# Performance work log

Hardware: AMD Instinct MI355X
Metric: run time of the kernel (lower is better)

## Reference

```python
import jax, jax.numpy as jnp
import numpy as np


def setup_inputs() -> dict:
    key = jax.random.key(0)
    k1, k2 = jax.random.split(key)
    B, L1, L2, D = 8, 2048, 2048, 1024
    features_1 = jax.random.normal(k1, (B, L1, D), dtype=jnp.float32)
    features_2 = jax.random.normal(k2, (B, L2, D), dtype=jnp.float32)
    return {"features_1": features_1, "features_2": features_2}


def reference(features_1, features_2):
    # similarity: [B, L1, L2], no scaling (matches original)
    sim = jnp.einsum("bmd,bnd->bmn", features_1, features_2)
    # both softmaxes in the original are dim=-1 (row softmax over L2)
    attn = jax.nn.softmax(sim, axis=-1)  # [B, L1, L2]
    attended_1 = jnp.einsum("bmn,bnd->bmd", attn, features_2)   # [B, L1, D]
    attended_2 = jnp.einsum("bmn,bmd->bnd", attn, features_1)   # attn^T @ f1 -> [B, L2, D]
    return (attended_1, attended_2)
```

## Files before the change

### kernel.cpp

```cpp
#include <hip/hip_runtime.h>
#include <hip/hip_fp16.h>

#define LDIM 2048
#define DDIM 1024
#define NB 8

typedef __attribute__((ext_vector_type(8))) _Float16 f16x8;
typedef __attribute__((ext_vector_type(4))) float f32x4;
typedef unsigned int u32;

#define MFMA16(a, b, c) __builtin_amdgcn_mfma_f32_16x16x32_f16(a, b, c, 0, 0, 0)

typedef const __attribute__((address_space(1))) u32* gas_t;
typedef __attribute__((address_space(3))) u32* las_t;

__device__ __forceinline__ void gl16(const _Float16* g, _Float16* l) {
  __builtin_amdgcn_global_load_lds((gas_t)g, (las_t)l, 16, 0, 0);
}

#define SBAR() __builtin_amdgcn_s_barrier()
#define VMCNT(n) asm volatile("s_waitcnt vmcnt(" #n ")" ::: "memory")
#define LGKM0 asm volatile("s_waitcnt lgkmcnt(0)" ::: "memory")
#define SCHED0 __builtin_amdgcn_sched_barrier(0)

template <int MH, int KS, int BB, class FS, class FW>
__device__ __forceinline__ void phase(const _Float16* sh, int base_a, int base_b,
                                      f32x4 (&acc)[2][4][4], FS stg, FW wt) {
  f16x8 af[4], bf[4];
#pragma unroll
  for (int mr = 0; mr < 4; ++mr)
    af[mr] = *(const f16x8*)&sh[BB * 32768 + KS * 8192 + MH * 2048 + base_a + mr * 512];
#pragma unroll
  for (int nr = 0; nr < 4; ++nr)
    bf[nr] = *(const f16x8*)&sh[BB * 32768 + 16384 + KS * 8192 + base_b + nr * 512];
  stg();
  wt();
  __builtin_amdgcn_s_barrier();
  LGKM0;
  SCHED0;
  __builtin_amdgcn_s_setprio(1);
#pragma unroll
  for (int mr = 0; mr < 4; ++mr)
#pragma unroll
    for (int nr = 0; nr < 4; ++nr)
      acc[MH][mr][nr] = MFMA16(af[mr], bf[nr], acc[MH][mr][nr]);
  __builtin_amdgcn_s_setprio(0);
  SCHED0;
  __builtin_amdgcn_s_barrier();
}

template <int LDA, int NT>
__device__ __forceinline__ void gemm8(const _Float16* __restrict__ Ab,
                                      const _Float16* __restrict__ Bb,
                                      _Float16* sh, f32x4 (&acc)[2][4][4]) {
  const int tid = threadIdx.x;
  const int lane = tid & 63, w = tid >> 6;
  const int wm = w >> 2, wn = w & 3;
  const int l15 = lane & 15, g4 = lane >> 4;

  const int sw = (l15 >> 1) & 3;
  const int chk = (g4 ^ sw) << 3;
  const int base_a = (wm * 128 + l15) * 32 + chk;
  const int base_b = (wn * 64 + l15) * 32 + chk;

  const int srow = tid >> 2;
  const int scg = (tid & 3) ^ ((srow >> 1) & 3);
  const _Float16* gA = Ab + (size_t)srow * LDA + scg * 8;
  const _Float16* gB = Bb + (size_t)srow * LDA + scg * 8;
  _Float16* lw = sh + w * 512;

  auto stgA = [&](int kt, int kh, int tb) {
    const _Float16* g = gA + (size_t)kt * 64 + kh * 32;
    _Float16* l = lw + tb * 32768 + kh * 8192;
    gl16(g, l);
    gl16(g + (size_t)128 * LDA, l + 4096);
  };
  auto stgB = [&](int kt, int kh, int tb) {
    const _Float16* g = gB + (size_t)kt * 64 + kh * 32;
    _Float16* l = lw + tb * 32768 + 16384 + kh * 8192;
    gl16(g, l);
    gl16(g + (size_t)128 * LDA, l + 4096);
  };

  stgA(0, 0, 0); stgB(0, 0, 0);
  stgA(0, 1, 0); stgB(0, 1, 0);
  stgA(1, 0, 1); stgB(1, 0, 1);
  VMCNT(8);
  SBAR();

  for (int t = 0; t + 3 < NT; t += 2) {
    phase<0, 0, 0>(sh, base_a, base_b, acc, [&] { stgA(t + 1, 1, 1); }, [] {});
    phase<1, 0, 0>(sh, base_a, base_b, acc, [&] { stgB(t + 1, 1, 1); }, [] { VMCNT(8); });
    phase<0, 1, 0>(sh, base_a, base_b, acc, [&] { stgA(t + 2, 0, 0); }, [] {});
    phase<1, 1, 0>(sh, base_a, base_b, acc, [&] { stgB(t + 2, 0, 0); }, [] { VMCNT(8); });
    phase<0, 0, 1>(sh, base_a, base_b, acc, [&] { stgA(t + 2, 1, 0); }, [] {});
    phase<1, 0, 1>(sh, base_a, base_b, acc, [&] { stgB(t + 2, 1, 0); }, [] { VMCNT(8); });
    phase<0, 1, 1>(sh, base_a, base_b, acc, [&] { stgA(t + 3, 0, 1); }, [] {});
    phase<1, 1, 1>(sh, base_a, base_b, acc, [&] { stgB(t + 3, 0, 1); }, [] { VMCNT(8); });
  }
  constexpr int T = NT - 2;
  phase<0, 0, 0>(sh, base_a, base_b, acc, [&] { stgA(T + 1, 1, 1); }, [] {});
  phase<1, 0, 0>(sh, base_a, base_b, acc, [&] { stgB(T + 1, 1, 1); }, [] { VMCNT(8); });
  phase<0, 1, 0>(sh, base_a, base_b, acc, [] {}, [] {});
  phase<1, 1, 0>(sh, base_a, base_b, acc, [] {}, [] { VMCNT(4); });
  phase<0, 0, 1>(sh, base_a, base_b, acc, [] {}, [] {});
  phase<1, 0, 1>(sh, base_a, base_b, acc, [] {}, [] { VMCNT(0); });
  phase<0, 1, 1>(sh, base_a, base_b, acc, [] {}, [] {});
  phase<1, 1, 1>(sh, base_a, base_b, acc, [] {}, [] {});
}

__global__ __launch_bounds__(256)
void k_prep(const float* __restrict__ F1, const float* __restrict__ F2,
            _Float16* __restrict__ H1, _Float16* __restrict__ H2,
            _Float16* __restrict__ H1T, _Float16* __restrict__ H2T) {
  __shared__ _Float16 sT[64][72];
  const int bid = blockIdx.x;
  const int inp = bid >> 12;
  const int rem = bid & 4095;
  const int b = rem >> 9, rt = (rem >> 4) & 31, ct = rem & 15;
  const int r0 = rt * 64, c0 = ct * 64;

  const float* F = (inp ? F2 : F1) + (size_t)b * LDIM * DDIM;
  _Float16* H = (inp ? H2 : H1) + (size_t)b * LDIM * DDIM;
  _Float16* HT = (inp ? H2T : H1T) + (size_t)b * DDIM * LDIM;

  const int t = threadIdx.x;
  const int row = t >> 2, seg = (t & 3) * 16;
  {
    const float* src = F + (size_t)(r0 + row) * DDIM + c0 + seg;
    float4 v0 = *(const float4*)(src), v1 = *(const float4*)(src + 4);
    float4 v2 = *(const float4*)(src + 8), v3 = *(const float4*)(src + 12);
    _Float16 h[16];
#pragma unroll
    for (int j = 0; j < 4; ++j) {
      h[j] = (_Float16)((&v0.x)[j]); h[4 + j] = (_Float16)((&v1.x)[j]);
      h[8 + j] = (_Float16)((&v2.x)[j]); h[12 + j] = (_Float16)((&v3.x)[j]);
    }
    _Float16* dst = H + (size_t)(r0 + row) * DDIM + c0 + seg;
#pragma unroll
    for (int j = 0; j < 16; ++j) dst[j] = h[j];
#pragma unroll
    for (int j = 0; j < 16; ++j) sT[seg + j][row] = h[j];
  }
  __syncthreads();
  {
    const int cloc = t >> 2, rseg = (t & 3) * 16;
    _Float16* dst = HT + (size_t)(c0 + cloc) * LDIM + r0 + rseg;
    *(uint4*)dst = *(const uint4*)&sT[cloc][rseg];
    *(uint4*)(dst + 8) = *(const uint4*)&sT[cloc][rseg + 8];
  }
}

__global__ __launch_bounds__(512, 2)
void k_qk(const _Float16* __restrict__ H1, const _Float16* __restrict__ H2,
          _Float16* __restrict__ P, float2* __restrict__ partials) {
  __shared__ _Float16 sh[65536];
  const int tid = threadIdx.x;
  const int lane = tid & 63, w = tid >> 6;
  const int wm = w >> 2, wn = w & 3;
  const int l15 = lane & 15, g4 = lane >> 4;

  const int nwg = gridDim.x;
  const int orig = blockIdx.x;
  const int idx = (orig & 7) * (nwg >> 3) + (orig >> 3);
  const int b = idx >> 6, mt = (idx >> 3) & 7, ntb = idx & 7;
  const int m0 = mt << 8, n0 = ntb << 8;

  f32x4 acc[2][4][4];
#pragma unroll
  for (int i = 0; i < 2; ++i)
#pragma unroll
    for (int j = 0; j < 4; ++j)
#pragma unroll
      for (int k = 0; k < 4; ++k) acc[i][j][k] = (f32x4){0.f, 0.f, 0.f, 0.f};

  gemm8<1024, 16>(H1 + (size_t)b * LDIM * DDIM + (size_t)m0 * DDIM,
                  H2 + (size_t)b * LDIM * DDIM + (size_t)n0 * DDIM, sh, acc);

  float* sred = (float*)sh;
  float* sredS = sred + 1024;
  __syncthreads();

#pragma unroll
  for (int mh = 0; mh < 2; ++mh)
#pragma unroll
    for (int mr = 0; mr < 4; ++mr)
#pragma unroll
      for (int r = 0; r < 4; ++r) {
        float v = fmaxf(fmaxf(acc[mh][mr][0][r], acc[mh][mr][1][r]),
                        fmaxf(acc[mh][mr][2][r], acc[mh][mr][3][r]));
        v = fmaxf(v, __shfl_xor(v, 1, 64));
        v = fmaxf(v, __shfl_xor(v, 2, 64));
        v = fmaxf(v, __shfl_xor(v, 4, 64));
        v = fmaxf(v, __shfl_xor(v, 8, 64));
        if (l15 == 0) sred[(wm * 128 + mh * 64 + mr * 16 + g4 * 4 + r) * 4 + wn] = v;
      }
  __syncthreads();

  _Float16* pOut = P + ((size_t)b << 22);
#pragma unroll
  for (int mh = 0; mh < 2; ++mh)
#pragma unroll
    for (int mr = 0; mr < 4; ++mr)
#pragma unroll
      for (int r = 0; r < 4; ++r) {
        const int row = wm * 128 + mh * 64 + mr * 16 + g4 * 4 + r;
        const float m = fmaxf(fmaxf(sred[row * 4], sred[row * 4 + 1]),
                              fmaxf(sred[row * 4 + 2], sred[row * 4 + 3]));
        float s = 0.f;
#pragma unroll
        for (int nr = 0; nr < 4; ++nr) {
          float p = __expf(acc[mh][mr][nr][r] - m);
          s += p;
          pOut[(size_t)(m0 + row) * LDIM + n0 + wn * 64 + nr * 16 + l15] = (_Float16)p;
        }
        s += __shfl_xor(s, 1, 64);
        s += __shfl_xor(s, 2, 64);
        s += __shfl_xor(s, 4, 64);
        s += __shfl_xor(s, 8, 64);
        if (l15 == 0) sredS[row * 4 + wn] = s;
      }
  __syncthreads();
  if (tid < 256) {
    const float m = fmaxf(fmaxf(sred[tid * 4], sred[tid * 4 + 1]),
                          fmaxf(sred[tid * 4 + 2], sred[tid * 4 + 3]));
    const float L = sredS[tid * 4] + sredS[tid * 4 + 1] + sredS[tid * 4 + 2] + sredS[tid * 4 + 3];
    partials[((size_t)(b * 8 + ntb) << 11) + m0 + tid] = make_float2(m, L);
  }
}

__global__ void k_merge(const float2* __restrict__ partials, float* __restrict__ factors) {
  const int t = blockIdx.x * 256 + threadIdx.x;
  if (t >= NB * LDIM) return;
  const int b = t >> 11, row = t & 2047;
  float2 p[8];
  float M = -1e30f;
#pragma unroll
  for (int i = 0; i < 8; ++i) {
    p[i] = partials[((size_t)(b * 8 + i) << 11) + row];
    M = fmaxf(M, p[i].x);
  }
  float L = 0.f;
#pragma unroll
  for (int i = 0; i < 8; ++i) L += p[i].y * __expf(p[i].x - M);
  const float inv = 1.0f / L;
#pragma unroll
  for (int i = 0; i < 8; ++i)
    factors[((size_t)(b * 8 + i) << 11) + row] = __expf(p[i].x - M) * inv;
}

__global__ __launch_bounds__(256)
void k_scale_t(_Float16* __restrict__ P, const float* __restrict__ factors,
               _Float16* __restrict__ PT) {
  __shared__ _Float16 sT[64][72];
  const int bid = blockIdx.x;
  const int b = bid >> 10, mt = (bid >> 5) & 31, nt = bid & 31;
  const int m0 = mt * 64, n0 = nt * 64;
  const int nblk = n0 >> 8;

  _Float16* p = P + ((size_t)b << 22);
  _Float16* pt = PT + ((size_t)b << 22);

  const int t = threadIdx.x;
  const int row = t >> 2, seg = (t & 3) * 16;
  {
    const float f = factors[((size_t)(b * 8 + nblk) << 11) + m0 + row];
    const _Float16 hf = (_Float16)f;
    _Float16* src = p + (size_t)(m0 + row) * LDIM + n0 + seg;
    f16x8 h0 = *(const f16x8*)src, h1 = *(const f16x8*)(src + 8);
#pragma unroll
    for (int j = 0; j < 8; ++j) { h0[j] *= hf; h1[j] *= hf; }
    *(f16x8*)src = h0;
    *(f16x8*)(src + 8) = h1;
#pragma unroll
    for (int j = 0; j < 8; ++j) { sT[seg + j][row] = h0[j]; sT[seg + 8 + j][row] = h1[j]; }
  }
  __syncthreads();
  {
    const int nloc = t >> 2, mseg = (t & 3) * 16;
    _Float16* dst = pt + (size_t)(n0 + nloc) * LDIM + m0 + mseg;
    *(uint4*)dst = *(const uint4*)&sT[nloc][mseg];
    *(uint4*)(dst + 8) = *(const uint4*)&sT[nloc][mseg + 8];
  }
}

__global__ __launch_bounds__(512, 2)
void k_gemm(const _Float16* __restrict__ A, const _Float16* __restrict__ B,
            float* __restrict__ C) {
  __shared__ _Float16 sh[65536];
  const int tid = threadIdx.x;
  const int lane = tid & 63, w = tid >> 6;
  const int wm = w >> 2, wn = w & 3;
  const int l15 = lane & 15, g4 = lane >> 4;

  const int nwg = gridDim.x;
  const int orig = blockIdx.x;
  const int idx = (orig & 7) * (nwg >> 3) + (orig >> 3);
  const int b = idx >> 5, mt = (idx >> 2) & 7, dt = idx & 3;
  const int m0 = mt << 8, d0 = dt << 8;

  f32x4 acc[2][4][4];
#pragma unroll
  for (int i = 0; i < 2; ++i)
#pragma unroll
    for (int j = 0; j < 4; ++j)
#pragma unroll
      for (int k = 0; k < 4; ++k) acc[i][j][k] = (f32x4){0.f, 0.f, 0.f, 0.f};

  gemm8<2048, 32>(A + ((size_t)b << 22) + (size_t)m0 * LDIM,
                  B + ((size_t)b << 21) + (size_t)d0 * LDIM, sh, acc);

  float* outp = C + (size_t)b * LDIM * DDIM;
#pragma unroll
  for (int mh = 0; mh < 2; ++mh)
#pragma unroll
    for (int mr = 0; mr < 4; ++mr)
#pragma unroll
      for (int nr = 0; nr < 4; ++nr)
#pragma unroll
        for (int r = 0; r < 4; ++r)
          outp[(size_t)(m0 + wm * 128 + mh * 64 + mr * 16 + g4 * 4 + r) * DDIM +
               d0 + wn * 64 + nr * 16 + l15] = acc[mh][mr][nr][r];
}

extern "C" void kernel_launch(void* const* d_in, const int* in_sizes, int n_in,
                              void* d_out, int out_size, void* d_ws, size_t ws_size,
                              hipStream_t stream) {
  const float* f1 = (const float*)d_in[0];
  const float* f2 = (const float*)d_in[1];
  float* out1 = (float*)d_out;
  float* out2 = out1 + (size_t)NB * LDIM * DDIM;

  char* ws = (char*)d_ws;
  _Float16* H1T = (_Float16*)(ws);
  _Float16* H2T = (_Float16*)(ws + 33554432ull);
  _Float16* P   = (_Float16*)(ws + 67108864ull);
  _Float16* PT  = (_Float16*)(ws + 134217728ull);
  _Float16* H1  = (_Float16*)(ws + 134217728ull);
  _Float16* H2  = (_Float16*)(ws + 167772160ull);
  float2* partials = (float2*)(ws + 201326592ull);
  float* factors   = (float*)(ws + 203423744ull);

  k_prep<<<dim3(8192), dim3(256), 0, stream>>>(f1, f2, H1, H2, H1T, H2T);
  k_qk<<<dim3(512), dim3(512), 0, stream>>>(H1, H2, P, partials);
  k_merge<<<dim3(64), dim3(256), 0, stream>>>(partials, factors);
  k_scale_t<<<dim3(8192), dim3(256), 0, stream>>>(P, factors, PT);
  k_gemm<<<dim3(256), dim3(512), 0, stream>>>(P, H2T, out1);
  k_gemm<<<dim3(256), dim3(512), 0, stream>>>(PT, H1T, out2);
}
```

Measured before the change: 293.3 us.

## Software-pipeline LDS fragment reads one phase ahead of MFMA in GEMM mainloop

Restructures the GEMM main loop so the LDS fragment reads for the next phase are issued before the MFMAs of the current phase, using double-buffered register fragments. This drops the per-phase lgkmcnt(0) wait and the second barrier per phase, which are meant to hide LDS latency behind matrix math. The global-to-LDS staging schedule is re-sequenced to match, with adjusted vmcnt waits. In exchange it uses more VGPRs and relies on the compiler to insert correct LDS waits, and the barrier reduction could introduce races on buffer reuse.

After: 287.7 us. Within noise of the previous version (-1.9%).

```diff
diff --git a/kernel.cpp b/kernel.cpp
--- a/kernel.cpp
+++ b/kernel.cpp
@@ -20,34 +20,28 @@
 
 #define SBAR() __builtin_amdgcn_s_barrier()
 #define VMCNT(n) asm volatile("s_waitcnt vmcnt(" #n ")" ::: "memory")
-#define LGKM0 asm volatile("s_waitcnt lgkmcnt(0)" ::: "memory")
 #define SCHED0 __builtin_amdgcn_sched_barrier(0)
 
-template <int MH, int KS, int BB, class FS, class FW>
-__device__ __forceinline__ void phase(const _Float16* sh, int base_a, int base_b,
-                                      f32x4 (&acc)[2][4][4], FS stg, FW wt) {
-  f16x8 af[4], bf[4];
-#pragma unroll
-  for (int mr = 0; mr < 4; ++mr)
-    af[mr] = *(const f16x8*)&sh[BB * 32768 + KS * 8192 + MH * 2048 + base_a + mr * 512];
-#pragma unroll
-  for (int nr = 0; nr < 4; ++nr)
-    bf[nr] = *(const f16x8*)&sh[BB * 32768 + 16384 + KS * 8192 + base_b + nr * 512];
-  stg();
-  wt();
-  __builtin_amdgcn_s_barrier();
-  LGKM0;
-  SCHED0;
-  __builtin_amdgcn_s_setprio(1);
-#pragma unroll
-  for (int mr = 0; mr < 4; ++mr)
-#pragma unroll
-    for (int nr = 0; nr < 4; ++nr)
-      acc[MH][mr][nr] = MFMA16(af[mr], bf[nr], acc[MH][mr][nr]);
-  __builtin_amdgcn_s_setprio(0);
-  SCHED0;
-  __builtin_amdgcn_s_barrier();
-}
+#define RD(AF, BF, MH, KS, BUF)                                                        \
+  do {                                                                                 \
+    _Pragma("unroll") for (int mr = 0; mr < 4; ++mr)                                   \
+        AF[mr] = *(const f16x8*)&sh[(BUF)*32768 + (KS)*8192 + (MH)*2048 + base_a +     \
+                                    mr * 512];                                         \
+    _Pragma("unroll") for (int nr = 0; nr < 4; ++nr)                                   \
+        BF[nr] = *(const f16x8*)&sh[(BUF)*32768 + 16384 + (KS)*8192 + base_b +         \
+                                    nr * 512];                                         \
+  } while (0)
+
+#define MM(AF, BF, MH)                                                                 \
+  do {                                                                                 \
+    SCHED0;                                                                            \
+    __builtin_amdgcn_s_setprio(1);                                                     \
+    _Pragma("unroll") for (int mr = 0; mr < 4; ++mr)                                   \
+        _Pragma("unroll") for (int nr = 0; nr < 4; ++nr)                               \
+            acc[MH][mr][nr] = MFMA16(AF[mr], BF[nr], acc[MH][mr][nr]);                 \
+    __builtin_amdgcn_s_setprio(0);                                                     \
+    SCHED0;                                                                            \
+  } while (0)
 
 template <int LDA, int NT>
 __device__ __forceinline__ void gemm8(const _Float16* __restrict__ Ab,
@@ -69,44 +63,42 @@
   const _Float16* gB = Bb + (size_t)srow * LDA + scg * 8;
   _Float16* lw = sh + w * 512;
 
-  auto stgA = [&](int kt, int kh, int tb) {
-    const _Float16* g = gA + (size_t)kt * 64 + kh * 32;
-    _Float16* l = lw + tb * 32768 + kh * 8192;
+  auto stg = [&](int T, int h, int buf) {
+    const _Float16* g = ((h & 1) ? gB : gA) + (size_t)T * 64 + (h >> 1) * 32;
+    _Float16* l = lw + buf * 32768 + (h & 1) * 16384 + (h >> 1) * 8192;
     gl16(g, l);
     gl16(g + (size_t)128 * LDA, l + 4096);
   };
-  auto stgB = [&](int kt, int kh, int tb) {
-    const _Float16* g = gB + (size_t)kt * 64 + kh * 32;
-    _Float16* l = lw + tb * 32768 + 16384 + kh * 8192;
-    gl16(g, l);
-    gl16(g + (size_t)128 * LDA, l + 4096);
-  };
-
-  stgA(0, 0, 0); stgB(0, 0, 0);
-  stgA(0, 1, 0); stgB(0, 1, 0);
-  stgA(1, 0, 1); stgB(1, 0, 1);
-  VMCNT(8);
+
+  f16x8 a0[4], b0[4], a1[4], b1[4];
+
+  stg(0, 0, 0); stg(0, 1, 0); stg(0, 2, 0); stg(0, 3, 0); stg(1, 0, 1);
+  VMCNT(6);
   SBAR();
-
-  for (int t = 0; t + 3 < NT; t += 2) {
-    phase<0, 0, 0>(sh, base_a, base_b, acc, [&] { stgA(t + 1, 1, 1); }, [] {});
-    phase<1, 0, 0>(sh, base_a, base_b, acc, [&] { stgB(t + 1, 1, 1); }, [] { VMCNT(8); });
-    phase<0, 1, 0>(sh, base_a, base_b, acc, [&] { stgA(t + 2, 0, 0); }, [] {});
-    phase<1, 1, 0>(sh, base_a, base_b, acc, [&] { stgB(t + 2, 0, 0); }, [] { VMCNT(8); });
-    phase<0, 0, 1>(sh, base_a, base_b, acc, [&] { stgA(t + 2, 1, 0); }, [] {});
-    phase<1, 0, 1>(sh, base_a, base_b, acc, [&] { stgB(t + 2, 1, 0); }, [] { VMCNT(8); });
-    phase<0, 1, 1>(sh, base_a, base_b, acc, [&] { stgA(t + 3, 0, 1); }, [] {});
-    phase<1, 1, 1>(sh, base_a, base_b, acc, [&] { stgB(t + 3, 0, 1); }, [] { VMCNT(8); });
-  }
-  constexpr int T = NT - 2;
-  phase<0, 0, 0>(sh, base_a, base_b, acc, [&] { stgA(T + 1, 1, 1); }, [] {});
-  phase<1, 0, 0>(sh, base_a, base_b, acc, [&] { stgB(T + 1, 1, 1); }, [] { VMCNT(8); });
-  phase<0, 1, 0>(sh, base_a, base_b, acc, [] {}, [] {});
-  phase<1, 1, 0>(sh, base_a, base_b, acc, [] {}, [] { VMCNT(4); });
-  phase<0, 0, 1>(sh, base_a, base_b, acc, [] {}, [] {});
-  phase<1, 0, 1>(sh, base_a, base_b, acc, [] {}, [] { VMCNT(0); });
-  phase<0, 1, 1>(sh, base_a, base_b, acc, [] {}, [] {});
-  phase<1, 1, 1>(sh, base_a, base_b, acc, [] {}, [] {});
+  RD(a0, b0, 0, 0, 0);
+
+  for (int p = 0; p < NT / 2 - 1; ++p) {
+    const int t1 = 2 * p + 1, t2 = 2 * p + 2, t3 = 2 * p + 3;
+    RD(a1, b1, 1, 0, 0); stg(t1, 1, 1); VMCNT(4); SBAR(); MM(a0, b0, 0);
+    RD(a0, b0, 0, 1, 0); stg(t1, 2, 1);            SBAR(); MM(a1, b1, 1);
+    RD(a1, b1, 1, 1, 0); stg(t1, 3, 1); VMCNT(4); SBAR(); MM(a0, b0, 0);
+    RD(a0, b0, 0, 0, 1); stg(t2, 0, 0);            SBAR(); MM(a1, b1, 1);
+    RD(a1, b1, 1, 0, 1); stg(t2, 1, 0); VMCNT(4); SBAR(); MM(a0, b0, 0);
+    RD(a0, b0, 0, 1, 1); stg(t2, 2, 0);            SBAR(); MM(a1, b1, 1);
+    RD(a1, b1, 1, 1, 1); stg(t2, 3, 0); VMCNT(4); SBAR(); MM(a0, b0, 0);
+    RD(a0, b0, 0, 0, 0); stg(t3, 0, 1);            SBAR(); MM(a1, b1, 1);
+  }
+  {
+    const int t1 = NT - 1;
+    RD(a1, b1, 1, 0, 0); stg(t1, 1, 1); VMCNT(4); SBAR(); MM(a0, b0, 0);
+    RD(a0, b0, 0, 1, 0); stg(t1, 2, 1);            SBAR(); MM(a1, b1, 1);
+    RD(a1, b1, 1, 1, 0); stg(t1, 3, 1); VMCNT(4); SBAR(); MM(a0, b0, 0);
+    RD(a0, b0, 0, 0, 1);                           SBAR(); MM(a1, b1, 1);
+    RD(a1, b1, 1, 0, 1);                VMCNT(0); SBAR(); MM(a0, b0, 0);
+    RD(a0, b0, 0, 1, 1);                           SBAR(); MM(a1, b1, 1);
+    RD(a1, b1, 1, 1, 1);                           SBAR(); MM(a0, b0, 0);
+                                                   SBAR(); MM(a1, b1, 1);
+  }
 }
 
 __global__ __launch_bounds__(256)
```

## Reuse B fragments across M-halves, relayout LDS tiles, vectorize prep stores

Applied to the files above, without the earlier changes.

The GEMM inner phase now loads B fragments once per K-slice and reuses them across both M-halves instead of reloading them, which halves LDS reads for B. The LDS tile layout and staging order are reorganized: stages are interleaved by operand and k-half, and the prefetch depth and vmcnt thresholds are adjusted to match. The prep kernel also writes fp16 output with two 16-byte vector stores instead of scalar stores. The cost is extra live VGPRs to keep bf across phases and a more delicate wait-count schedule.

After: 290.0 us. No clear change (-1.1%).

```diff
diff --git a/kernel.cpp b/kernel.cpp
--- a/kernel.cpp
+++ b/kernel.cpp
@@ -23,16 +23,19 @@
 #define LGKM0 asm volatile("s_waitcnt lgkmcnt(0)" ::: "memory")
 #define SCHED0 __builtin_amdgcn_sched_barrier(0)
 
-template <int MH, int KS, int BB, class FS, class FW>
-__device__ __forceinline__ void phase(const _Float16* sh, int base_a, int base_b,
-                                      f32x4 (&acc)[2][4][4], FS stg, FW wt) {
-  f16x8 af[4], bf[4];
+template <int MH, int KS, int BUF, bool RB, class FS, class FW>
+__device__ __forceinline__ void ph(const _Float16* sh, int base_a, int base_b,
+                                   f16x8 (&bf)[4], f32x4 (&acc)[2][4][4], FS stg, FW wt) {
+  f16x8 af[4];
+  if (RB) {
+#pragma unroll
+    for (int nr = 0; nr < 4; ++nr)
+      bf[nr] = *(const f16x8*)&sh[BUF * 32768 + KS * 4096 + base_b + nr * 512];
+  }
 #pragma unroll
   for (int mr = 0; mr < 4; ++mr)
-    af[mr] = *(const f16x8*)&sh[BB * 32768 + KS * 8192 + MH * 2048 + base_a + mr * 512];
-#pragma unroll
-  for (int nr = 0; nr < 4; ++nr)
-    bf[nr] = *(const f16x8*)&sh[BB * 32768 + 16384 + KS * 8192 + base_b + nr * 512];
+    af[mr] = *(const f16x8*)&sh[BUF * 32768 + KS * 4096 + MH * 2048 + base_a + mr * 512];
+  SCHED0;
   stg();
   wt();
   __builtin_amdgcn_s_barrier();
@@ -58,10 +61,9 @@
   const int wm = w >> 2, wn = w & 3;
   const int l15 = lane & 15, g4 = lane >> 4;
 
-  const int sw = (l15 >> 1) & 3;
-  const int chk = (g4 ^ sw) << 3;
-  const int base_a = (wm * 128 + l15) * 32 + chk;
-  const int base_b = (wn * 64 + l15) * 32 + chk;
+  const int chk = (g4 ^ ((l15 >> 1) & 3)) << 3;
+  const int base_a = wm * 8192 + l15 * 32 + chk;
+  const int base_b = 16384 + (wn >> 1) * 8192 + ((wn & 1) * 64 + l15) * 32 + chk;
 
   const int srow = tid >> 2;
   const int scg = (tid & 3) ^ ((srow >> 1) & 3);
@@ -69,44 +71,41 @@
   const _Float16* gB = Bb + (size_t)srow * LDA + scg * 8;
   _Float16* lw = sh + w * 512;
 
-  auto stgA = [&](int kt, int kh, int tb) {
-    const _Float16* g = gA + (size_t)kt * 64 + kh * 32;
-    _Float16* l = lw + tb * 32768 + kh * 8192;
+  auto stg = [&](int T, int op, int kh) {
+    const _Float16* g = (op ? gB : gA) + (size_t)T * 64 + kh * 32;
+    _Float16* l = lw + (T & 1) * 32768 + op * 16384 + kh * 4096;
     gl16(g, l);
-    gl16(g + (size_t)128 * LDA, l + 4096);
+    gl16(g + (size_t)128 * LDA, l + 8192);
   };
-  auto stgB = [&](int kt, int kh, int tb) {
-    const _Float16* g = gB + (size_t)kt * 64 + kh * 32;
-    _Float16* l = lw + tb * 32768 + 16384 + kh * 8192;
-    gl16(g, l);
-    gl16(g + (size_t)128 * LDA, l + 4096);
-  };
-
-  stgA(0, 0, 0); stgB(0, 0, 0);
-  stgA(0, 1, 0); stgB(0, 1, 0);
-  stgA(1, 0, 1); stgB(1, 0, 1);
-  VMCNT(8);
+
+  f16x8 bf[4];
+
+  stg(0, 1, 0); stg(0, 0, 0); stg(0, 1, 1); stg(0, 0, 1);
+  stg(1, 1, 0); stg(1, 0, 0); stg(1, 1, 1);
+  VMCNT(6);
   SBAR();
 
-  for (int t = 0; t + 3 < NT; t += 2) {
-    phase<0, 0, 0>(sh, base_a, base_b, acc, [&] { stgA(t + 1, 1, 1); }, [] {});
-    phase<1, 0, 0>(sh, base_a, base_b, acc, [&] { stgB(t + 1, 1, 1); }, [] { VMCNT(8); });
-    phase<0, 1, 0>(sh, base_a, base_b, acc, [&] { stgA(t + 2, 0, 0); }, [] {});
-    phase<1, 1, 0>(sh, base_a, base_b, acc, [&] { stgB(t + 2, 0, 0); }, [] { VMCNT(8); });
-    phase<0, 0, 1>(sh, base_a, base_b, acc, [&] { stgA(t + 2, 1, 0); }, [] {});
-    phase<1, 0, 1>(sh, base_a, base_b, acc, [&] { stgB(t + 2, 1, 0); }, [] { VMCNT(8); });
-    phase<0, 1, 1>(sh, base_a, base_b, acc, [&] { stgA(t + 3, 0, 1); }, [] {});
-    phase<1, 1, 1>(sh, base_a, base_b, acc, [&] { stgB(t + 3, 0, 1); }, [] { VMCNT(8); });
-  }
-  constexpr int T = NT - 2;
-  phase<0, 0, 0>(sh, base_a, base_b, acc, [&] { stgA(T + 1, 1, 1); }, [] {});
-  phase<1, 0, 0>(sh, base_a, base_b, acc, [&] { stgB(T + 1, 1, 1); }, [] { VMCNT(8); });
-  phase<0, 1, 0>(sh, base_a, base_b, acc, [] {}, [] {});
-  phase<1, 1, 0>(sh, base_a, base_b, acc, [] {}, [] { VMCNT(4); });
-  phase<0, 0, 1>(sh, base_a, base_b, acc, [] {}, [] {});
-  phase<1, 0, 1>(sh, base_a, base_b, acc, [] {}, [] { VMCNT(0); });
-  phase<0, 1, 1>(sh, base_a, base_b, acc, [] {}, [] {});
-  phase<1, 1, 1>(sh, base_a, base_b, acc, [] {}, [] {});
+  for (int i = 0; i < NT / 2 - 1; ++i) {
+    const int T1 = 2 * i + 1, T2 = 2 * i + 2, T3 = 2 * i + 3;
+    ph<0, 0, 0, true >(sh, base_a, base_b, bf, acc, [&] { stg(T1, 0, 1); }, [] {});
+    ph<1, 0, 0, false>(sh, base_a, base_b, bf, acc, [&] { stg(T2, 1, 0); }, [] {});
+    ph<0, 1, 0, true >(sh, base_a, base_b, bf, acc, [&] { stg(T2, 0, 0); }, [] {});
+    ph<1, 1, 0, false>(sh, base_a, base_b, bf, acc, [&] { stg(T2, 1, 1); }, [] { VMCNT(6); });
+    ph<0, 0, 1, true >(sh, base_a, base_b, bf, acc, [&] { stg(T2, 0, 1); }, [] {});
+    ph<1, 0, 1, false>(sh, base_a, base_b, bf, acc, [&] { stg(T3, 1, 0); }, [] {});
+    ph<0, 1, 1, true >(sh, base_a, base_b, bf, acc, [&] { stg(T3, 0, 0); }, [] {});
+    ph<1, 1, 1, false>(sh, base_a, base_b, bf, acc, [&] { stg(T3, 1, 1); }, [] { VMCNT(6); });
+  }
+  {
+    ph<0, 0, 0, true >(sh, base_a, base_b, bf, acc, [&] { stg(NT - 1, 0, 1); }, [] {});
+    ph<1, 0, 0, false>(sh, base_a, base_b, bf, acc, [] {}, [] {});
+    ph<0, 1, 0, true >(sh, base_a, base_b, bf, acc, [] {}, [] {});
+    ph<1, 1, 0, false>(sh, base_a, base_b, bf, acc, [] {}, [] { VMCNT(0); });
+    ph<0, 0, 1, true >(sh, base_a, base_b, bf, acc, [] {}, [] {});
+    ph<1, 0, 1, false>(sh, base_a, base_b, bf, acc, [] {}, [] {});
+    ph<0, 1, 1, true >(sh, base_a, base_b, bf, acc, [] {}, [] {});
+    ph<1, 1, 1, false>(sh, base_a, base_b, bf, acc, [] {}, [] {});
+  }
 }
 
 __global__ __launch_bounds__(256)
@@ -130,17 +129,17 @@
     const float* src = F + (size_t)(r0 + row) * DDIM + c0 + seg;
     float4 v0 = *(const float4*)(src), v1 = *(const float4*)(src + 4);
     float4 v2 = *(const float4*)(src + 8), v3 = *(const float4*)(src + 12);
-    _Float16 h[16];
+    f16x8 ha, hb;
 #pragma unroll
     for (int j = 0; j < 4; ++j) {
-      h[j] = (_Float16)((&v0.x)[j]); h[4 + j] = (_Float16)((&v1.x)[j]);
-      h[8 + j] = (_Float16)((&v2.x)[j]); h[12 + j] = (_Float16)((&v3.x)[j]);
+      ha[j] = (_Float16)((&v0.x)[j]); ha[4 + j] = (_Float16)((&v1.x)[j]);
+      hb[j] = (_Float16)((&v2.x)[j]); hb[4 + j] = (_Float16)((&v3.x)[j]);
     }
     _Float16* dst = H + (size_t)(r0 + row) * DDIM + c0 + seg;
-#pragma unroll
-    for (int j = 0; j < 16; ++j) dst[j] = h[j];
-#pragma unroll
-    for (int j = 0; j < 16; ++j) sT[seg + j][row] = h[j];
+    *(f16x8*)dst = ha;
+    *(f16x8*)(dst + 8) = hb;
+#pragma unroll
+    for (int j = 0; j < 8; ++j) { sT[seg + j][row] = ha[j]; sT[seg + 8 + j][row] = hb[j]; }
   }
   __syncthreads();
   {
```
